# Performance work log

Measured on AMD Instinct MI355X. Metric: run time of the kernel, lower is better.

## Reference

```python
import jax, jax.numpy as jnp
import numpy as np

B, N, Q, D = 1, 6, 10000, 256
HEADS, LEVELS, NPTS, ZANCH = 8, 1, 8, 4  # NPTS = 2*n_points, ZANCH = num_points_in_pillar
HF, WF = 32, 88
HD = D // HEADS


def setup_inputs() -> dict:
    key = jax.random.key(0)
    ks = jax.random.split(key, 18)
    s = 1.0 / np.sqrt(D)
    inp = {
        'queries': jax.random.normal(ks[0], (B, N, Q, D), jnp.float32),
        'pos_emb': jax.random.normal(ks[1], (B, N, Q, D), jnp.float32),
        'lvl_emb': jax.random.normal(ks[2], (LEVELS, D), jnp.float32),
        'cam_emb': jax.random.normal(ks[3], (N, D), jnp.float32),
        'features0': jax.random.normal(ks[4], (B * N, D, HF, WF), jnp.float32),
        'reference_points_3D': jax.random.uniform(ks[5], (B, N, Q, ZANCH, 2), jnp.float32),
        'bev_mask': jax.random.randint(ks[6], (B, N, Q, ZANCH, 2), 0, 2).astype(bool),
        # MSDeformAttn3D params
        'W_value': jax.random.normal(ks[7], (D, D), jnp.float32) * s,
        'b_value': jnp.zeros((D,), jnp.float32),
        'W_off': jax.random.normal(ks[8], (HEADS * LEVELS * NPTS * 2, D), jnp.float32) * 0.01,
        'b_off': jax.random.uniform(ks[9], (HEADS * LEVELS * NPTS * 2,), jnp.float32, -2.0, 2.0),
        'W_attn': jax.random.normal(ks[10], (HEADS * LEVELS * NPTS, D), jnp.float32) * s,
        'b_attn': jnp.zeros((HEADS * LEVELS * NPTS,), jnp.float32),
        'W_inner': jax.random.normal(ks[11], (D, D), jnp.float32) * s,
        'b_inner': jnp.zeros((D,), jnp.float32),
        # SpatialCrossAttention.output_proj
        'W_out': jax.random.normal(ks[12], (D, D), jnp.float32) * s,
        'b_out': jnp.zeros((D,), jnp.float32),
    }
    return inp


def _bilinear(value_t, loc, H, W):
    # value_t: (bn, heads, H*W, hd); loc: (bn, q, heads, pts, 2) normalized to [0,1]
    bn, q, heads, pts, _ = loc.shape
    hd = value_t.shape[-1]
    # grid_sample(2*loc-1, align_corners=False) -> pixel coord = loc*size - 0.5
    x = loc[..., 0] * W - 0.5
    y = loc[..., 1] * H - 0.5
    x0 = jnp.floor(x); y0 = jnp.floor(y)
    dx = x - x0; dy = y - y0
    x0 = x0.astype(jnp.int32); y0 = y0.astype(jnp.int32)
    out = jnp.zeros((bn, heads, q * pts, hd), value_t.dtype)
    corners = ((0, 0, (1 - dx) * (1 - dy)), (1, 0, dx * (1 - dy)),
               (0, 1, (1 - dx) * dy), (1, 1, dx * dy))
    for ox, oy, w in corners:
        xi = x0 + ox; yi = y0 + oy
        valid = (xi >= 0) & (xi < W) & (yi >= 0) & (yi < H)  # zero padding
        wgt = jnp.where(valid, w, 0.0)
        idx = jnp.clip(yi, 0, H - 1) * W + jnp.clip(xi, 0, W - 1)  # (bn,q,heads,pts)
        idx_t = idx.transpose(0, 2, 1, 3).reshape(bn, heads, q * pts)
        g = jnp.take_along_axis(value_t, idx_t[..., None], axis=2)  # (bn,heads,q*pts,hd)
        wgt_t = wgt.transpose(0, 2, 1, 3).reshape(bn, heads, q * pts)
        out = out + g * wgt_t[..., None]
    return out.reshape(bn, heads, q, pts, hd)


def _forward(queries, pos_emb, lvl_emb, cam_emb, features0, reference_points_3D, bev_mask,
             W_value, b_value, W_off, b_off, W_attn, b_attn, W_inner, b_inner, W_out, b_out):
    b, n, q, d = queries.shape
    hf, wf = features0.shape[-2:]
    # flatten features + level/cam embeddings -> (b*n, hw, d)
    feat = features0.reshape(b, n, d, hf * wf)
    feat = feat + lvl_emb[0][None, None, :, None] + cam_emb[None, :, :, None]
    input_flatten = feat.transpose(0, 1, 3, 2).reshape(b * n, hf * wf, d)

    qp = (queries + pos_emb).reshape(b * n, q, d)
    ref = reference_points_3D.reshape(b * n, q, ZANCH, 2)

    # --- MSDeformAttn3D (single level) ---
    value = (input_flatten @ W_value.T + b_value).reshape(b * n, hf * wf, HEADS, HD)
    off = (qp @ W_off.T + b_off).reshape(b * n, q, HEADS, LEVELS, NPTS, 2)
    attw = jax.nn.softmax((qp @ W_attn.T + b_attn).reshape(b * n, q, HEADS, LEVELS * NPTS), axis=-1)
    attw = attw.reshape(b * n, q, HEADS, LEVELS, NPTS)
    normalizer = jnp.array([wf, hf], queries.dtype)  # (W, H)
    pts_per_z = NPTS // ZANCH
    off_z = off.reshape(b * n, q, HEADS, LEVELS, pts_per_z, ZANCH, 2)
    loc = ref[:, :, None, None, None, :, :] + off_z / normalizer
    loc = loc.reshape(b * n, q, HEADS, LEVELS, NPTS, 2)

    value_t = value.transpose(0, 2, 1, 3)  # (bn, heads, hw, hd)
    sampled = _bilinear(value_t, loc[:, :, :, 0], hf, wf)  # (bn,heads,q,pts,hd)
    attw_t = attw[:, :, :, 0].transpose(0, 2, 1, 3)  # (bn,heads,q,pts)
    out = jnp.einsum('bhqp,bhqpc->bqhc', attw_t, sampled).reshape(b * n, q, d)
    out = out @ W_inner.T + b_inner

    # --- scatter back per camera, normalize by hit count ---
    attn = out.reshape(b, n, q, d)
    # indexes come from batch 0's mask (as in the original code)
    hit = (bev_mask[0, :, :, :, 0].astype(jnp.int32).sum(-1) > 0).astype(queries.dtype)  # (n,q)
    slots = (attn * hit[None, :, :, None]).sum(1)  # (b,q,d)
    count = (bev_mask[..., 0].astype(jnp.int32).sum(-1) > 0).astype(queries.dtype).sum(1)
    count = jnp.clip(count, 1.0, None)  # (b,q)
    slots = slots / count[..., None]
    return slots @ W_out.T + b_out


def reference(queries, pos_emb, lvl_emb, cam_emb, features0, reference_points_3D, bev_mask,
              W_value, b_value, W_off, b_off, W_attn, b_attn, W_inner, b_inner, W_out, b_out):
    return _forward(queries, pos_emb, lvl_emb, cam_emb, features0, reference_points_3D, bev_mask,
                    W_value, b_value, W_off, b_off, W_attn, b_attn, W_inner, b_inner, W_out, b_out)
```

## Files before the change

### kernel.cpp

```cpp
#include <hip/hip_runtime.h>
#include <hip/hip_bf16.h>

#define BN     6
#define NQ     10000
#define DIM    256
#define HEADS  8
#define HDD    32
#define HF_    32
#define WF_    88
#define HW_    (HF_*WF_)
#define MTOT   (BN*NQ)

typedef __attribute__((ext_vector_type(8))) unsigned short ushort8_t;
typedef __attribute__((ext_vector_type(8))) short bf16x8;
typedef __attribute__((ext_vector_type(4))) float f32x4;

static __device__ inline unsigned short f2bf(float x) {
    __hip_bfloat16 b = __float2bfloat16(x);
    return *(unsigned short*)&b;
}

__global__ __launch_bounds__(256)
void k_wcvt(const float* __restrict__ Wv, const float* __restrict__ Wo,
            const float* __restrict__ Wa, const float* __restrict__ Wi,
            const float* __restrict__ Wz,
            unsigned short* __restrict__ Wv_bf, unsigned short* __restrict__ Woa_bf,
            unsigned short* __restrict__ Wi_bf, unsigned short* __restrict__ Wz_bf)
{
    const int i4 = (blockIdx.x*256 + threadIdx.x) * 4;
    if (i4 < 65536) {
        float4 v;
        ushort4 p;
        v = *(const float4*)(Wv+i4); p.x=f2bf(v.x);p.y=f2bf(v.y);p.z=f2bf(v.z);p.w=f2bf(v.w);
        *(ushort4*)(Wv_bf+i4) = p;
        v = *(const float4*)(Wi+i4); p.x=f2bf(v.x);p.y=f2bf(v.y);p.z=f2bf(v.z);p.w=f2bf(v.w);
        *(ushort4*)(Wi_bf+i4) = p;
        v = *(const float4*)(Wz+i4); p.x=f2bf(v.x);p.y=f2bf(v.y);p.z=f2bf(v.z);p.w=f2bf(v.w);
        *(ushort4*)(Wz_bf+i4) = p;
    }
    if (i4 < 32768) {
        float4 v = *(const float4*)(Wo+i4);
        ushort4 p; p.x=f2bf(v.x);p.y=f2bf(v.y);p.z=f2bf(v.z);p.w=f2bf(v.w);
        *(ushort4*)(Woa_bf+i4) = p;
    }
    if (i4 < 16384) {
        float4 v = *(const float4*)(Wa+i4);
        ushort4 p; p.x=f2bf(v.x);p.y=f2bf(v.y);p.z=f2bf(v.z);p.w=f2bf(v.w);
        *(ushort4*)(Woa_bf+32768+i4) = p;
    }
}

__global__ __launch_bounds__(256)
void k_ebias(const float* __restrict__ lvl, const float* __restrict__ cam,
             const float* __restrict__ Wv, const float* __restrict__ bv,
             float* __restrict__ ebias)
{
    const int n = blockIdx.x;
    const int j = threadIdx.x;
    __shared__ float e[DIM];
    e[j] = lvl[j] + cam[n*DIM + j];
    __syncthreads();
    const float* w = Wv + (size_t)j*DIM;
    float s = bv[j];
    for (int d = 0; d < DIM; ++d) s += e[d]*w[d];
    ebias[n*DIM + j] = s;
}

__global__ __launch_bounds__(256)
void k_mask(const int* __restrict__ bev, float* __restrict__ hitf,
            float* __restrict__ scale, float* __restrict__ biasf)
{
    const int q = blockIdx.x*256 + threadIdx.x;
    if (q >= NQ) return;
    float cnt = 0.f;
    #pragma unroll
    for (int n = 0; n < BN; ++n) {
        int hit = 0;
        #pragma unroll
        for (int z = 0; z < 4; ++z)
            hit |= (bev[(((size_t)n*NQ + q)*4 + z)*2] != 0);
        hitf[(size_t)n*NQ + q] = (float)hit;
        cnt += (float)hit;
    }
    biasf[q] = (cnt > 0.f) ? 1.f : 0.f;
    scale[q] = 1.f / fmaxf(cnt, 1.f);
}

__global__ __launch_bounds__(256)
void k_feat(const float* __restrict__ feat, unsigned short* __restrict__ featT)
{
    __shared__ float Tf[64][68];
    const int cam = blockIdx.z;
    const int d0 = blockIdx.y * 64;
    const int p0 = blockIdx.x * 64;
    const int tid = threadIdx.x;
    #pragma unroll
    for (int i = 0; i < 4; ++i) {
        const int d = (tid>>4) + i*16;
        const int p4 = (tid&15)*4;
        *(float4*)&Tf[d][p4] = *(const float4*)(feat + ((size_t)cam*DIM + d0 + d)*HW_ + p0 + p4);
    }
    __syncthreads();
    const int p = tid>>2, dq = tid&3;
    unsigned short* ob = featT + ((size_t)cam*HW_ + p0 + p)*DIM + d0;
    #pragma unroll
    for (int i = 0; i < 4; ++i) {
        const int d4 = dq*4 + i*16;
        ushort4 pk;
        pk.x = f2bf(Tf[d4+0][p]); pk.y = f2bf(Tf[d4+1][p]);
        pk.z = f2bf(Tf[d4+2][p]); pk.w = f2bf(Tf[d4+3][p]);
        *(ushort4*)(ob + d4) = pk;
    }
}

__global__ __launch_bounds__(256)
void k_value_mfma(const unsigned short* __restrict__ featT,
                  const unsigned short* __restrict__ Wv_bf,
                  const float* __restrict__ ebias,
                  unsigned short* __restrict__ value_bf)
{
    __shared__ unsigned short Ap[128][72];
    __shared__ unsigned short Bc[64][72];
    const int cam = blockIdx.z;
    const int p0 = blockIdx.x * 128;
    const int c0 = blockIdx.y * 64;
    const int tid = threadIdx.x;
    const int lane = tid & 63, wave = tid >> 6;
    const int quad = lane >> 4, l15 = lane & 15;
    f32x4 acc[2][4] = {};
    const unsigned short* fbase = featT + ((size_t)cam*HW_ + p0)*DIM;

    for (int k0 = 0; k0 < DIM; k0 += 64) {
        #pragma unroll
        for (int i = 0; i < 4; ++i) {
            const int row = (tid>>3) + i*32;
            const int k8 = (tid&7)*8;
            *(ushort8_t*)&Ap[row][k8] = *(const ushort8_t*)(fbase + (size_t)row*DIM + k0 + k8);
        }
        #pragma unroll
        for (int i = 0; i < 2; ++i) {
            const int row = (tid>>3) + i*32;
            const int k8 = (tid&7)*8;
            *(ushort8_t*)&Bc[row][k8] = *(const ushort8_t*)(Wv_bf + (size_t)(c0+row)*DIM + k0 + k8);
        }
        __syncthreads();
        #pragma unroll
        for (int s = 0; s < 2; ++s) {
            const int kf = s*32 + quad*8;
            bf16x8 a[2], b[4];
            #pragma unroll
            for (int mt = 0; mt < 2; ++mt)
                a[mt] = *(const bf16x8*)&Ap[(wave*2+mt)*16 + l15][kf];
            #pragma unroll
            for (int nt = 0; nt < 4; ++nt)
                b[nt] = *(const bf16x8*)&Bc[nt*16 + l15][kf];
            #pragma unroll
            for (int mt = 0; mt < 2; ++mt)
                #pragma unroll
                for (int nt = 0; nt < 4; ++nt)
                    acc[mt][nt] = __builtin_amdgcn_mfma_f32_16x16x32_bf16(a[mt], b[nt], acc[mt][nt], 0,0,0);
        }
        __syncthreads();
    }
    #pragma unroll
    for (int nt = 0; nt < 4; ++nt) {
        const int c = c0 + nt*16 + l15;
        const float eb = ebias[cam*DIM + c];
        const int h = c >> 5, cc = c & 31;
        unsigned short* vb = value_bf + (size_t)(cam*HEADS + h)*HW_*HDD + cc;
        #pragma unroll
        for (int mt = 0; mt < 2; ++mt)
            #pragma unroll
            for (int r = 0; r < 4; ++r) {
                const int p = p0 + (wave*2+mt)*16 + quad*4 + r;
                vb[(size_t)p*HDD] = f2bf(acc[mt][nt][r] + eb);
            }
    }
}

__global__ __launch_bounds__(256)
void k_qpcvt(const float* __restrict__ Qr, const float* __restrict__ Pe,
             unsigned short* __restrict__ QP)
{
    const size_t total = (size_t)MTOT*DIM/8;
    for (size_t i = (size_t)blockIdx.x*256 + threadIdx.x; i < total;
         i += (size_t)gridDim.x*256) {
        const float4 x0 = ((const float4*)Qr)[i*2+0];
        const float4 x1 = ((const float4*)Qr)[i*2+1];
        const float4 y0 = ((const float4*)Pe)[i*2+0];
        const float4 y1 = ((const float4*)Pe)[i*2+1];
        ushort8_t o;
        o[0]=f2bf(x0.x+y0.x); o[1]=f2bf(x0.y+y0.y);
        o[2]=f2bf(x0.z+y0.z); o[3]=f2bf(x0.w+y0.w);
        o[4]=f2bf(x1.x+y1.x); o[5]=f2bf(x1.y+y1.y);
        o[6]=f2bf(x1.z+y1.z); o[7]=f2bf(x1.w+y1.w);
        ((ushort8_t*)QP)[i] = o;
    }
}

__global__ __launch_bounds__(256, 4)
void k_offattn(const unsigned short* __restrict__ QP,
               const unsigned short* __restrict__ Woa_bf,
               const float* __restrict__ boff, const float* __restrict__ battn,
               float* __restrict__ off_ws, float* __restrict__ attw_ws)
{
    const int m0 = blockIdx.x * 32;
    const int tid = threadIdx.x;
    const int lane = tid & 63, wave = tid >> 6;
    const int quad = lane >> 4, l15 = lane & 15;
    const int n0 = wave * 48;
    f32x4 acc[2][3] = {};

    const unsigned short* abase0 = QP + (size_t)(m0 + l15)*DIM;
    const unsigned short* abase1 = QP + (size_t)(m0 + 16 + l15)*DIM;
    const unsigned short* wbase[3];
    #pragma unroll
    for (int nt = 0; nt < 3; ++nt)
        wbase[nt] = Woa_bf + (size_t)(n0 + nt*16 + l15)*DIM;

    #pragma unroll
    for (int kc = 0; kc < 8; ++kc) {
        const int kk = kc*32 + quad*8;
        const bf16x8 a0 = *(const bf16x8*)(abase0 + kk);
        const bf16x8 a1 = *(const bf16x8*)(abase1 + kk);
        bf16x8 b[3];
        #pragma unroll
        for (int nt = 0; nt < 3; ++nt)
            b[nt] = *(const bf16x8*)(wbase[nt] + kk);
        #pragma unroll
        for (int nt = 0; nt < 3; ++nt) {
            acc[0][nt] = __builtin_amdgcn_mfma_f32_16x16x32_bf16(a0, b[nt], acc[0][nt], 0,0,0);
            acc[1][nt] = __builtin_amdgcn_mfma_f32_16x16x32_bf16(a1, b[nt], acc[1][nt], 0,0,0);
        }
    }

    #pragma unroll
    for (int nt = 0; nt < 3; ++nt) {
        const int col = n0 + nt*16 + l15;
        const float bias = (col < 128) ? boff[col] : battn[col-128];
        #pragma unroll
        for (int mt = 0; mt < 2; ++mt) {
            #pragma unroll
            for (int r = 0; r < 4; ++r) {
                const int m = m0 + mt*16 + quad*4 + r;
                const float v = acc[mt][nt][r] + bias;
                if (col < 128) off_ws [(size_t)m*128 + col]       = v;
                else           attw_ws[(size_t)m*64 + (col-128)]  = v;
            }
        }
    }
}

__global__ __launch_bounds__(256)
void k_sample(const unsigned short* __restrict__ value_bf,
              const float* __restrict__ off_ws, const float* __restrict__ attw_ws,
              const float* __restrict__ ref3d, const float* __restrict__ hitf,
              const float* __restrict__ scale, unsigned short* __restrict__ asum_bf)
{
    const int q0 = blockIdx.x * 8;
    const int tid = threadIdx.x;

    __shared__ float s_off[8][128];
    __shared__ float s_att[8][64];
    __shared__ float s_ref[8][8];
    __shared__ float s_hit[BN][8];
    __shared__ float s_scl[8];

    if (tid < 48) s_hit[tid>>3][tid&7] = hitf[(size_t)(tid>>3)*NQ + q0 + (tid&7)];
    if (tid < 8)  s_scl[tid] = scale[q0 + tid];

    const int quarter = tid & 3;
    const int h  = (tid >> 2) & 7;
    const int ql = tid >> 5;

    float acc[8];
    #pragma unroll
    for (int c = 0; c < 8; ++c) acc[c] = 0.f;

    for (int n = 0; n < BN; ++n) {
        __syncthreads();
        {
            const float4* so = (const float4*)(off_ws + ((size_t)n*NQ + q0)*128);
            ((float4*)&s_off[0][0])[tid] = so[tid];
            const float2* sa = (const float2*)(attw_ws + ((size_t)n*NQ + q0)*64);
            ((float2*)&s_att[0][0])[tid] = sa[tid];
            if (tid < 64)
                (&s_ref[0][0])[tid] = (ref3d + ((size_t)n*NQ + q0)*8)[tid];
        }
        __syncthreads();

        if (s_hit[n][ql] != 0.f) {
            float lg[8];
            float mx = -1e30f;
            #pragma unroll
            for (int p = 0; p < 8; ++p) { lg[p] = s_att[ql][h*8+p]; mx = fmaxf(mx, lg[p]); }
            float ssum = 0.f;
            #pragma unroll
            for (int p = 0; p < 8; ++p) { lg[p] = __expf(lg[p]-mx); ssum += lg[p]; }
            const float inv = 1.f/ssum;

            const unsigned short* vbase =
                value_bf + (size_t)(n*HEADS + h)*HW_*HDD + quarter*8;

            #pragma unroll
            for (int p = 0; p < 8; ++p) {
                const int z = p & 3;
                const float ax = s_ref[ql][z*2+0]*WF_ + s_off[ql][h*16+p*2+0] - 0.5f;
                const float ay = s_ref[ql][z*2+1]*HF_ + s_off[ql][h*16+p*2+1] - 0.5f;
                const float fx = floorf(ax), fy = floorf(ay);
                const float dx = ax-fx, dy = ay-fy;
                const int x0 = (int)fx, y0 = (int)fy;
                const float wp = lg[p]*inv;
                #pragma unroll
                for (int oy = 0; oy < 2; ++oy) {
                    const int yi = y0 + oy;
                    const float wy = oy ? dy : 1.f-dy;
                    #pragma unroll
                    for (int ox = 0; ox < 2; ++ox) {
                        const int xi = x0 + ox;
                        const float wx = ox ? dx : 1.f-dx;
                        const bool valid = ((unsigned)xi < WF_) & ((unsigned)yi < HF_);
                        const float cw = valid ? wp*wy*wx : 0.f;
                        const int xc = min(max(xi, 0), WF_-1);
                        const int yc = min(max(yi, 0), HF_-1);
                        const ushort8_t v = *(const ushort8_t*)(vbase + (size_t)(yc*WF_ + xc)*HDD);
                        #pragma unroll
                        for (int c = 0; c < 8; ++c)
                            acc[c] += cw * __uint_as_float(((unsigned)v[c]) << 16);
                    }
                }
            }
        }
    }

    const float sc = s_scl[ql];
    ushort8_t o;
    #pragma unroll
    for (int c = 0; c < 8; ++c) o[c] = f2bf(acc[c]*sc);
    *(ushort8_t*)(asum_bf + ((size_t)(q0+ql))*DIM + h*HDD + quarter*8) = o;
}

__global__ __launch_bounds__(256)
void k_gemm_mfma(const unsigned short* __restrict__ A_bf,
                 const unsigned short* __restrict__ W_bf,
                 const float* __restrict__ bias, const float* __restrict__ rowscale,
                 float* __restrict__ out_f, unsigned short* __restrict__ out_b, int M)
{
    __shared__ unsigned short As[128][72];
    __shared__ unsigned short Bs[64][72];
    const int m0 = blockIdx.x * 128;
    const int j0 = blockIdx.y * 64;
    const int tid = threadIdx.x;
    const int lane = tid & 63, wave = tid >> 6;
    const int quad = lane >> 4, l15 = lane & 15;
    f32x4 acc[2][4] = {};

    for (int k0 = 0; k0 < DIM; k0 += 64) {
        #pragma unroll
        for (int i = 0; i < 4; ++i) {
            const int row = (tid>>3) + i*32;
            const int k8 = (tid&7)*8;
            ushort8_t v = {0,0,0,0,0,0,0,0};
            if (m0 + row < M)
                v = *(const ushort8_t*)(A_bf + (size_t)(m0+row)*DIM + k0 + k8);
            *(ushort8_t*)&As[row][k8] = v;
        }
        #pragma unroll
        for (int i = 0; i < 2; ++i) {
            const int row = (tid>>3) + i*32;
            const int k8 = (tid&7)*8;
            *(ushort8_t*)&Bs[row][k8] = *(const ushort8_t*)(W_bf + (size_t)(j0+row)*DIM + k0 + k8);
        }
        __syncthreads();
        #pragma unroll
        for (int s = 0; s < 2; ++s) {
            const int kf = s*32 + quad*8;
            bf16x8 a[2], b[4];
            #pragma unroll
            for (int mt = 0; mt < 2; ++mt)
                a[mt] = *(const bf16x8*)&As[(wave*2+mt)*16 + l15][kf];
            #pragma unroll
            for (int nt = 0; nt < 4; ++nt)
                b[nt] = *(const bf16x8*)&Bs[nt*16 + l15][kf];
            #pragma unroll
            for (int mt = 0; mt < 2; ++mt)
                #pragma unroll
                for (int nt = 0; nt < 4; ++nt)
                    acc[mt][nt] = __builtin_amdgcn_mfma_f32_16x16x32_bf16(a[mt], b[nt], acc[mt][nt], 0,0,0);
        }
        __syncthreads();
    }
    #pragma unroll
    for (int nt = 0; nt < 4; ++nt) {
        const int j = j0 + nt*16 + l15;
        const float bj = bias[j];
        #pragma unroll
        for (int mt = 0; mt < 2; ++mt) {
            #pragma unroll
            for (int r = 0; r < 4; ++r) {
                const int m = m0 + (wave*2+mt)*16 + quad*4 + r;
                if (m >= M) continue;
                const float f = rowscale ? rowscale[m] : 1.f;
                const float v = acc[mt][nt][r] + f*bj;
                if (out_f) out_f[(size_t)m*DIM + j] = v;
                if (out_b) out_b[(size_t)m*DIM + j] = f2bf(v);
            }
        }
    }
}

extern "C" void kernel_launch(void* const* d_in, const int* in_sizes, int n_in,
                              void* d_out, int out_size, void* d_ws, size_t ws_size,
                              hipStream_t stream)
{
    const float* queries = (const float*)d_in[0];
    const float* pos_emb = (const float*)d_in[1];
    const float* lvl_emb = (const float*)d_in[2];
    const float* cam_emb = (const float*)d_in[3];
    const float* features= (const float*)d_in[4];
    const float* ref3d   = (const float*)d_in[5];
    const int*   bev     = (const int*)d_in[6];
    const float* Wv = (const float*)d_in[7];
    const float* bv = (const float*)d_in[8];
    const float* Wo = (const float*)d_in[9];
    const float* bo = (const float*)d_in[10];
    const float* Wa = (const float*)d_in[11];
    const float* ba = (const float*)d_in[12];
    const float* Wi = (const float*)d_in[13];
    const float* bi = (const float*)d_in[14];
    const float* Wz = (const float*)d_in[15];
    const float* bz = (const float*)d_in[16];
    float* out = (float*)d_out;

    char* ws = (char*)d_ws;
    size_t o = 0;
    auto alloc = [&](size_t bytes) { char* p = ws + o; o += (bytes + 255) & ~size_t(255); return p; };
    unsigned short* value_bf = (unsigned short*)alloc((size_t)BN*HEADS*HW_*HDD*2);
    unsigned short* featT    = (unsigned short*)alloc((size_t)BN*HW_*DIM*2);
    float* off_ws   = (float*)alloc((size_t)MTOT*128*4);
    float* attw_ws  = (float*)alloc((size_t)MTOT*64*4);
    unsigned short* QP_bf    = (unsigned short*)alloc((size_t)MTOT*DIM*2);
    unsigned short* asum_bf  = (unsigned short*)alloc((size_t)NQ*DIM*2);
    unsigned short* slots_bf = (unsigned short*)alloc((size_t)NQ*DIM*2);
    unsigned short* Wv_bf  = (unsigned short*)alloc(65536*2);
    unsigned short* Woa_bf = (unsigned short*)alloc(49152*2);
    unsigned short* Wi_bf  = (unsigned short*)alloc(65536*2);
    unsigned short* Wz_bf  = (unsigned short*)alloc(65536*2);
    float* hitf   = (float*)alloc((size_t)BN*NQ*4);
    float* scalev = (float*)alloc(NQ*4);
    float* biasf  = (float*)alloc(NQ*4);
    float* ebias  = (float*)alloc(BN*DIM*4);

    k_wcvt  <<<64, 256, 0, stream>>>(Wv, Wo, Wa, Wi, Wz, Wv_bf, Woa_bf, Wi_bf, Wz_bf);
    k_ebias <<<BN, 256, 0, stream>>>(lvl_emb, cam_emb, Wv, bv, ebias);
    k_mask  <<<(NQ+255)/256, 256, 0, stream>>>(bev, hitf, scalev, biasf);
    k_feat  <<<dim3(HW_/64, DIM/64, BN), 256, 0, stream>>>(features, featT);
    k_value_mfma<<<dim3(HW_/128, DIM/64, BN), 256, 0, stream>>>(featT, Wv_bf, ebias, value_bf);
    k_qpcvt <<<2048, 256, 0, stream>>>(queries, pos_emb, QP_bf);
    k_offattn<<<MTOT/32, 256, 0, stream>>>(QP_bf, Woa_bf, bo, ba, off_ws, attw_ws);
    k_sample <<<NQ/8, 256, 0, stream>>>(value_bf, off_ws, attw_ws, ref3d, hitf, scalev, asum_bf);
    k_gemm_mfma<<<dim3((NQ+127)/128, DIM/64), 256, 0, stream>>>(asum_bf, Wi_bf, bi, biasf, nullptr, slots_bf, NQ);
    k_gemm_mfma<<<dim3((NQ+127)/128, DIM/64), 256, 0, stream>>>(slots_bf, Wz_bf, bz, nullptr, out, nullptr, NQ);
}
```

Before: 360.5 us.

## Remap sampling kernel: one wavefront per query, split points and cameras across lanes

```diff
diff --git a/kernel.cpp b/kernel.cpp
--- a/kernel.cpp
+++ b/kernel.cpp
@@ -257,87 +257,100 @@
               const float* __restrict__ ref3d, const float* __restrict__ hitf,
               const float* __restrict__ scale, unsigned short* __restrict__ asum_bf)
 {
-    const int q0 = blockIdx.x * 8;
-    const int tid = threadIdx.x;
-
-    __shared__ float s_off[8][128];
-    __shared__ float s_att[8][64];
-    __shared__ float s_ref[8][8];
-    __shared__ float s_hit[BN][8];
-    __shared__ float s_scl[8];
-
-    if (tid < 48) s_hit[tid>>3][tid&7] = hitf[(size_t)(tid>>3)*NQ + q0 + (tid&7)];
-    if (tid < 8)  s_scl[tid] = scale[q0 + tid];
-
-    const int quarter = tid & 3;
-    const int h  = (tid >> 2) & 7;
-    const int ql = tid >> 5;
-
-    float acc[8];
-    #pragma unroll
-    for (int c = 0; c < 8; ++c) acc[c] = 0.f;
-
-    for (int n = 0; n < BN; ++n) {
-        __syncthreads();
-        {
-            const float4* so = (const float4*)(off_ws + ((size_t)n*NQ + q0)*128);
-            ((float4*)&s_off[0][0])[tid] = so[tid];
-            const float2* sa = (const float2*)(attw_ws + ((size_t)n*NQ + q0)*64);
-            ((float2*)&s_att[0][0])[tid] = sa[tid];
-            if (tid < 64)
-                (&s_ref[0][0])[tid] = (ref3d + ((size_t)n*NQ + q0)*8)[tid];
-        }
-        __syncthreads();
-
-        if (s_hit[n][ql] != 0.f) {
-            float lg[8];
-            float mx = -1e30f;
-            #pragma unroll
-            for (int p = 0; p < 8; ++p) { lg[p] = s_att[ql][h*8+p]; mx = fmaxf(mx, lg[p]); }
-            float ssum = 0.f;
-            #pragma unroll
-            for (int p = 0; p < 8; ++p) { lg[p] = __expf(lg[p]-mx); ssum += lg[p]; }
-            const float inv = 1.f/ssum;
-
-            const unsigned short* vbase =
-                value_bf + (size_t)(n*HEADS + h)*HW_*HDD + quarter*8;
-
-            #pragma unroll
-            for (int p = 0; p < 8; ++p) {
-                const int z = p & 3;
-                const float ax = s_ref[ql][z*2+0]*WF_ + s_off[ql][h*16+p*2+0] - 0.5f;
-                const float ay = s_ref[ql][z*2+1]*HF_ + s_off[ql][h*16+p*2+1] - 0.5f;
-                const float fx = floorf(ax), fy = floorf(ay);
-                const float dx = ax-fx, dy = ay-fy;
-                const int x0 = (int)fx, y0 = (int)fy;
-                const float wp = lg[p]*inv;
+    const int q    = blockIdx.x*4 + (threadIdx.x >> 6);
+    const int lane = threadIdx.x & 63;
+    const int ch2  = lane >> 5;
+    const int quarter = (lane >> 3) & 3;
+    const int h    = lane & 7;
+
+    float acc[32];
+    #pragma unroll
+    for (int c = 0; c < 32; ++c) acc[c] = 0.f;
+
+    #pragma unroll
+    for (int i = 0; i < 3; ++i) {
+        const int n = ch2*3 + i;
+        const int m = n*NQ + q;
+        if (hitf[m] == 0.f) continue;
+
+        const float4 l0 = *(const float4*)(attw_ws + (size_t)m*64 + h*8);
+        const float4 l1 = *(const float4*)(attw_ws + (size_t)m*64 + h*8 + 4);
+        const float mx = fmaxf(fmaxf(fmaxf(l0.x,l0.y),fmaxf(l0.z,l0.w)),
+                               fmaxf(fmaxf(l1.x,l1.y),fmaxf(l1.z,l1.w)));
+        const float e0 = __expf(l0.x-mx), e1 = __expf(l0.y-mx);
+        const float e2 = __expf(l0.z-mx), e3 = __expf(l0.w-mx);
+        const float e4 = __expf(l1.x-mx), e5 = __expf(l1.y-mx);
+        const float e6 = __expf(l1.z-mx), e7 = __expf(l1.w-mx);
+        const float inv = 1.f/(e0+e1+e2+e3+e4+e5+e6+e7);
+        float wa = (quarter&2) ? ((quarter&1)? e6 : e4) : ((quarter&1)? e2 : e0);
+        float wb = (quarter&2) ? ((quarter&1)? e7 : e5) : ((quarter&1)? e3 : e1);
+        wa *= inv; wb *= inv;
+
+        const float4 of = *(const float4*)(off_ws + (size_t)m*128 + h*16 + quarter*4);
+        const float4 rr = *(const float4*)(ref3d + (size_t)m*8 + (quarter&1)*4);
+
+        const unsigned short* vbase = value_bf + (size_t)(n*HEADS + h)*HW_*HDD;
+
+        #pragma unroll
+        for (int j = 0; j < 2; ++j) {
+            const float ww = j ? wb : wa;
+            const float ax = (j ? rr.z : rr.x)*WF_ + (j ? of.z : of.x) - 0.5f;
+            const float ay = (j ? rr.w : rr.y)*HF_ + (j ? of.w : of.y) - 0.5f;
+            const float fx = floorf(ax), fy = floorf(ay);
+            const float dx = ax-fx, dy = ay-fy;
+            const int x0 = (int)fx, y0 = (int)fy;
+            #pragma unroll
+            for (int oy = 0; oy < 2; ++oy) {
+                const int yi = y0 + oy;
+                const float wy = oy ? dy : 1.f-dy;
                 #pragma unroll
-                for (int oy = 0; oy < 2; ++oy) {
-                    const int yi = y0 + oy;
-                    const float wy = oy ? dy : 1.f-dy;
+                for (int ox = 0; ox < 2; ++ox) {
+                    const int xi = x0 + ox;
+                    const float wx = ox ? dx : 1.f-dx;
+                    const bool valid = ((unsigned)xi < WF_) & ((unsigned)yi < HF_);
+                    const float cw = valid ? ww*wy*wx : 0.f;
+                    const int pix = min(max(yi,0),HF_-1)*WF_ + min(max(xi,0),WF_-1);
+                    const unsigned short* vp = vbase + pix*HDD;
+                    const ushort8_t v0 = *(const ushort8_t*)(vp);
+                    const ushort8_t v1 = *(const ushort8_t*)(vp + 8);
+                    const ushort8_t v2 = *(const ushort8_t*)(vp + 16);
+                    const ushort8_t v3 = *(const ushort8_t*)(vp + 24);
                     #pragma unroll
-                    for (int ox = 0; ox < 2; ++ox) {
-                        const int xi = x0 + ox;
-                        const float wx = ox ? dx : 1.f-dx;
-                        const bool valid = ((unsigned)xi < WF_) & ((unsigned)yi < HF_);
-                        const float cw = valid ? wp*wy*wx : 0.f;
-                        const int xc = min(max(xi, 0), WF_-1);
-                        const int yc = min(max(yi, 0), HF_-1);
-                        const ushort8_t v = *(const ushort8_t*)(vbase + (size_t)(yc*WF_ + xc)*HDD);
-                        #pragma unroll
-                        for (int c = 0; c < 8; ++c)
-                            acc[c] += cw * __uint_as_float(((unsigned)v[c]) << 16);
+                    for (int c = 0; c < 8; ++c) {
+                        acc[c]    += cw*__uint_as_float(((unsigned)v0[c])<<16);
+                        acc[8+c]  += cw*__uint_as_float(((unsigned)v1[c])<<16);
+                        acc[16+c] += cw*__uint_as_float(((unsigned)v2[c])<<16);
+                        acc[24+c] += cw*__uint_as_float(((unsigned)v3[c])<<16);
                     }
                 }
             }
         }
     }
 
-    const float sc = s_scl[ql];
-    ushort8_t o;
-    #pragma unroll
-    for (int c = 0; c < 8; ++c) o[c] = f2bf(acc[c]*sc);
-    *(ushort8_t*)(asum_bf + ((size_t)(q0+ql))*DIM + h*HDD + quarter*8) = o;
+    #pragma unroll
+    for (int c = 0; c < 32; ++c) {
+        acc[c] += __shfl_xor(acc[c], 8, 64);
+        acc[c] += __shfl_xor(acc[c], 16, 64);
+        acc[c] += __shfl_xor(acc[c], 32, 64);
+    }
+
+    if ((lane & 56) == 0) {
+        const float sc = scale[q];
+        unsigned short* ob = asum_bf + (size_t)q*DIM + h*HDD;
+        ushort8_t o;
+        #pragma unroll
+        for (int c = 0; c < 8; ++c) o[c] = f2bf(acc[c]*sc);
+        *(ushort8_t*)(ob) = o;
+        #pragma unroll
+        for (int c = 0; c < 8; ++c) o[c] = f2bf(acc[8+c]*sc);
+        *(ushort8_t*)(ob + 8) = o;
+        #pragma unroll
+        for (int c = 0; c < 8; ++c) o[c] = f2bf(acc[16+c]*sc);
+        *(ushort8_t*)(ob + 16) = o;
+        #pragma unroll
+        for (int c = 0; c < 8; ++c) o[c] = f2bf(acc[24+c]*sc);
+        *(ushort8_t*)(ob + 24) = o;
+    }
 }
 
 __global__ __launch_bounds__(256)
@@ -458,7 +471,7 @@
     k_value_mfma<<<dim3(HW_/128, DIM/64, BN), 256, 0, stream>>>(featT, Wv_bf, ebias, value_bf);
     k_qpcvt <<<2048, 256, 0, stream>>>(queries, pos_emb, QP_bf);
     k_offattn<<<MTOT/32, 256, 0, stream>>>(QP_bf, Woa_bf, bo, ba, off_ws, attw_ws);
-    k_sample <<<NQ/8, 256, 0, stream>>>(value_bf, off_ws, attw_ws, ref3d, hitf, scalev, asum_bf);
+    k_sample <<<NQ/4, 256, 0, stream>>>(value_bf, off_ws, attw_ws, ref3d, hitf, scalev, asum_bf);
     k_gemm_mfma<<<dim3((NQ+127)/128, DIM/64), 256, 0, stream>>>(asum_bf, Wi_bf, bi, biasf, nullptr, slots_bf, NQ);
     k_gemm_mfma<<<dim3((NQ+127)/128, DIM/64), 256, 0, stream>>>(slots_bf, Wz_bf, bz, nullptr, out, nullptr, NQ);
 }
```

Result: slower. 500.2 us (+38.8%).
